# Kernel optimization log

Hardware: AMD Instinct MI355X
Metric: run time of the kernel (lower is better)

Reference implementation:

```python
import math
import jax, jax.numpy as jnp
import numpy as np

IMAGE_SIZE = 224


def _resize_bilinear(img, out_h, out_w):
    """PyTorch F.interpolate(mode='bilinear', align_corners=False) equivalent.
    img: [B, H, W] -> [B, out_h, out_w]. No antialiasing (matches torch default)."""
    B, H, W = img.shape

    def coords(out, size):
        r = jnp.maximum((jnp.arange(out, dtype=jnp.float32) + 0.5) * (size / out) - 0.5, 0.0)
        i0 = jnp.minimum(jnp.floor(r).astype(jnp.int32), size - 1)
        i1 = jnp.minimum(i0 + 1, size - 1)
        w = r - i0.astype(jnp.float32)
        return i0, i1, w

    r0, r1, wr = coords(out_h, H)
    c0, c1, wc = coords(out_w, W)
    rows = img[:, r0, :] * (1.0 - wr)[None, :, None] + img[:, r1, :] * wr[None, :, None]
    out = rows[:, :, c0] * (1.0 - wc)[None, None, :] + rows[:, :, c1] * wc[None, None, :]
    return out


def _normalize_minmax(x, eps=1e-8):
    mn = x.min()
    mx = x.max()
    return jnp.where(mx - mn < eps, jnp.zeros_like(x), (x - mn) / (mx - mn + eps))


def _grid_embed(vals, n):
    """Row-major scatter of vals[:, :n] into a ceil(sqrt(n))^2 grid (zero padded)."""
    B = vals.shape[0]
    gs = int(math.ceil(math.sqrt(n)))
    pad = gs * gs - n
    return jnp.pad(vals, ((0, 0), (0, pad))).reshape(B, gs, gs)


def setup_inputs() -> dict:
    key = jax.random.key(0)
    hidden_state = jax.random.normal(key, (32, 512, 4096, 1), dtype=jnp.float32)
    return {"hidden_state": hidden_state}


def reference(hidden_state):
    B, E, N, _ = hidden_state.shape
    x = hidden_state[..., 0]  # [B, E, N]

    # temporal view: mean over nodes -> [B, E] -> grid -> resize
    t_grid = _grid_embed(x.mean(axis=2), E)
    temporal = _normalize_minmax(_resize_bilinear(t_grid, IMAGE_SIZE, IMAGE_SIZE))

    # spatial view: mean over embedding dim -> [B, N] -> grid -> resize
    s_grid = _grid_embed(x.mean(axis=1), N)
    spatial = _normalize_minmax(_resize_bilinear(s_grid, IMAGE_SIZE, IMAGE_SIZE))

    # correlation view: row-normalized centered features, [B, E, E] correlation
    xc = x - x.mean(axis=2, keepdims=True)
    xn = xc / (jnp.linalg.norm(xc, axis=2, keepdims=True) + 1e-8)
    corr = jnp.einsum('bin,bjn->bij', xn, xn)  # [B, E, E]
    correlation = _normalize_minmax(_resize_bilinear(corr, IMAGE_SIZE, IMAGE_SIZE))

    # [B, 3, image_size, image_size]
    return jnp.stack([temporal, spatial, correlation], axis=1)
```

## Files before the change

### kernel.cpp

```cpp
#include <hip/hip_runtime.h>
#include <hip/hip_bf16.h>
#include <math.h>

#define IMG 224
#define PIX (IMG*IMG)
#define B_ 32
#define E_ 512
#define N_ 4096
#define SV_BLOCKS 256

typedef __attribute__((ext_vector_type(8))) short bf16x8;
typedef __attribute__((ext_vector_type(4))) float f32x4;

__device__ inline unsigned short f2bf(float f){
  unsigned u = __float_as_uint(f);
  unsigned r = (u + 0x7FFFu + ((u >> 16) & 1u)) >> 16;
  return (unsigned short)r;
}
__device__ inline float wave_sum(float v){
  #pragma unroll
  for (int o = 32; o; o >>= 1) v += __shfl_down(v, o);
  return v;
}

__global__ void __launch_bounds__(256) stats_fused(const float* __restrict__ x,
                                                   float* __restrict__ meanv,
                                                   float* __restrict__ rnormv,
                                                   float* __restrict__ colpart){
  int b = blockIdx.x >> 4, chunk = blockIdx.x & 15;
  int e0 = chunk << 5;
  const float* xb = x + ((size_t)b * E_ + e0) * N_;
  int t = threadIdx.x;
  float csum[16];
  #pragma unroll
  for (int k = 0; k < 16; k++) csum[k] = 0.f;
  __shared__ float red[16];
  float4 v[4];
  const float4* xr0 = (const float4*)xb;
  #pragma unroll
  for (int k = 0; k < 4; k++) v[k] = xr0[t + 256 * k];
  for (int e = 0; e < 32; e++){
    float s = 0.f, ss = 0.f;
    #pragma unroll
    for (int k = 0; k < 4; k++){
      float4 w = v[k];
      csum[4*k+0] += w.x; csum[4*k+1] += w.y;
      csum[4*k+2] += w.z; csum[4*k+3] += w.w;
      s  += w.x + w.y + w.z + w.w;
      ss += w.x*w.x + w.y*w.y + w.z*w.z + w.w*w.w;
    }
    if (e < 31){
      const float4* nx = (const float4*)(xb + (size_t)(e + 1) * N_);
      #pragma unroll
      for (int k = 0; k < 4; k++) v[k] = nx[t + 256 * k];
    }
    float sw = wave_sum(s), ssw = wave_sum(ss);
    int wv = t >> 6, ln = t & 63;
    __syncthreads();
    if (ln == 0){ red[wv] = sw; red[8 + wv] = ssw; }
    __syncthreads();
    if (t == 0){
      float S  = red[0] + red[1] + red[2] + red[3];
      float SS = red[8] + red[9] + red[10] + red[11];
      float mu = S * (1.f / N_);
      float var = fmaxf(SS - S * S * (1.f / N_), 0.f);
      meanv [b * E_ + e0 + e] = mu;
      rnormv[b * E_ + e0 + e] = 1.f / (sqrtf(var) + 1e-8f);
    }
  }
  float* cp = colpart + ((size_t)(b * 16 + chunk)) * N_;
  #pragma unroll
  for (int k = 0; k < 4; k++){
    float4 o;
    o.x = csum[4*k+0]; o.y = csum[4*k+1]; o.z = csum[4*k+2]; o.w = csum[4*k+3];
    *(float4*)(cp + 1024 * k + 4 * t) = o;
  }
}

__global__ void __launch_bounds__(256) col_finalize(const float* __restrict__ colpart,
                                                    float* __restrict__ colmean){
  int b = blockIdx.x >> 4;
  int n = ((blockIdx.x & 15) << 8) + threadIdx.x;
  float s = 0.f;
  #pragma unroll
  for (int c = 0; c < 16; c++) s += colpart[((size_t)(b * 16 + c)) * N_ + n];
  colmean[b * N_ + n] = s * (1.f / E_);
}

__device__ inline float grid_val(const float* v, int gs, int n, int r, int c){
  int idx = r * gs + c;
  return (idx < n) ? v[idx] : 0.f;
}
__device__ inline float bilin(const float* v, int gs, int n, int i, int j){
  float sc = (float)((double)gs / 224.0);
  float r = fmaxf(((float)i + 0.5f) * sc - 0.5f, 0.f);
  float c = fmaxf(((float)j + 0.5f) * sc - 0.5f, 0.f);
  int r0 = min((int)r, gs - 1), c0 = min((int)c, gs - 1);
  int r1 = min(r0 + 1, gs - 1), c1 = min(c0 + 1, gs - 1);
  float wr = r - (float)r0, wc = c - (float)c0;
  float v00 = grid_val(v, gs, n, r0, c0), v10 = grid_val(v, gs, n, r1, c0);
  float v01 = grid_val(v, gs, n, r0, c1), v11 = grid_val(v, gs, n, r1, c1);
  float ra = v00 * (1.f - wr) + v10 * wr;
  float rb = v01 * (1.f - wr) + v11 * wr;
  return ra * (1.f - wc) + rb * wc;
}

__global__ void __launch_bounds__(256) small_views(const float* __restrict__ meanv,
                                                   const float* __restrict__ colmean,
                                                   float* __restrict__ out,
                                                   float* __restrict__ scr){
  float tmn = INFINITY, tmx = -INFINITY, smn = INFINITY, smx = -INFINITY;
  for (int g = blockIdx.x * 256 + threadIdx.x; g < B_ * PIX; g += SV_BLOCKS * 256){
    int b = g / PIX, p = g - b * PIX;
    int i = p / IMG, j = p - i * IMG;
    float tv = bilin(meanv   + b * E_, 23, E_, i, j);
    float sv = bilin(colmean + b * N_, 64, N_, i, j);
    out[((size_t)b * 3 + 0) * PIX + p] = tv;
    out[((size_t)b * 3 + 1) * PIX + p] = sv;
    tmn = fminf(tmn, tv); tmx = fmaxf(tmx, tv);
    smn = fminf(smn, sv); smx = fmaxf(smx, sv);
  }
  #pragma unroll
  for (int o = 32; o; o >>= 1){
    tmn = fminf(tmn, __shfl_down(tmn, o)); tmx = fmaxf(tmx, __shfl_down(tmx, o));
    smn = fminf(smn, __shfl_down(smn, o)); smx = fmaxf(smx, __shfl_down(smx, o));
  }
  __shared__ float red[4][4];
  int wv = threadIdx.x >> 6, ln = threadIdx.x & 63;
  if (ln == 0){ red[wv][0] = tmn; red[wv][1] = tmx; red[wv][2] = smn; red[wv][3] = smx; }
  __syncthreads();
  if (threadIdx.x == 0){
    scr[blockIdx.x * 4 + 0] = fminf(fminf(red[0][0], red[1][0]), fminf(red[2][0], red[3][0]));
    scr[blockIdx.x * 4 + 1] = fmaxf(fmaxf(red[0][1], red[1][1]), fmaxf(red[2][1], red[3][1]));
    scr[blockIdx.x * 4 + 2] = fminf(fminf(red[0][2], red[1][2]), fminf(red[2][2], red[3][2]));
    scr[blockIdx.x * 4 + 3] = fmaxf(fmaxf(red[0][3], red[1][3]), fmaxf(red[2][3], red[3][3]));
  }
}

__global__ void __launch_bounds__(256) build_y(const float* __restrict__ x,
                                               const float* __restrict__ meanv,
                                               const float* __restrict__ rnormv,
                                               ushort* __restrict__ y, int b0){
  int bb = blockIdx.x / IMG;
  int i  = blockIdx.x % IMG;
  int b  = b0 + bb;
  float sc = (float)(512.0 / 224.0);
  float r = fmaxf(((float)i + 0.5f) * sc - 0.5f, 0.f);
  int r0 = min((int)r, E_ - 1);
  int r1 = min(r0 + 1, E_ - 1);
  float w = r - (float)r0;
  float rn0 = rnormv[b * E_ + r0], rn1 = rnormv[b * E_ + r1];
  float m0  = meanv [b * E_ + r0], m1  = meanv [b * E_ + r1];
  float a0 = (1.f - w) * rn0, a1 = w * rn1;
  float cc = -(a0 * m0 + a1 * m1);
  const float* x0 = x + ((size_t)b * E_ + r0) * N_;
  const float* x1 = x + ((size_t)b * E_ + r1) * N_;
  ushort* yo = y + ((size_t)bb * IMG + i) * N_;
  int c0 = threadIdx.x * 16;
  __align__(16) ushort tmp[16];
  #pragma unroll
  for (int q = 0; q < 4; q++){
    float4 v0 = *(const float4*)(x0 + c0 + q * 4);
    float4 v1 = *(const float4*)(x1 + c0 + q * 4);
    tmp[q * 4 + 0] = f2bf(a0 * v0.x + a1 * v1.x + cc);
    tmp[q * 4 + 1] = f2bf(a0 * v0.y + a1 * v1.y + cc);
    tmp[q * 4 + 2] = f2bf(a0 * v0.z + a1 * v1.z + cc);
    tmp[q * 4 + 3] = f2bf(a0 * v0.w + a1 * v1.w + cc);
  }
  *(int4*)(yo + c0)     = *(int4*)(tmp);
  *(int4*)(yo + c0 + 8) = *(int4*)(tmp + 8);
}

#define LDSTR 72
__global__ void __launch_bounds__(256) corr_gemm(const ushort* __restrict__ y,
                                                 float* __restrict__ out,
                                                 float* __restrict__ scr, int b0){
  int bb = blockIdx.x >> 4;
  int tile = blockIdx.x & 15;
  int ti = tile >> 2, tj = tile & 3;
  int b = b0 + bb;
  const ushort* yb = y + (size_t)bb * IMG * N_;
  __shared__ ushort lA[64 * LDSTR];
  __shared__ ushort lB[64 * LDSTR];
  int t = threadIdx.x;
  int wv = t >> 6, ln = t & 63;
  int wm = wv & 1, wn = wv >> 1;
  int quad = ln >> 4, l16 = ln & 15;
  f32x4 acc[2][2] = {};
  int s = t & 7, r2 = t >> 3;
  int rA0 = min(ti * 64 + r2,      223), rA1 = min(ti * 64 + r2 + 32, 223);
  int rB0 = min(tj * 64 + r2,      223), rB1 = min(tj * 64 + r2 + 32, 223);
  for (int k0 = 0; k0 < N_; k0 += 64){
    int4 a0 = *(const int4*)(yb + (size_t)rA0 * N_ + k0 + s * 8);
    int4 a1 = *(const int4*)(yb + (size_t)rA1 * N_ + k0 + s * 8);
    int4 b0v = *(const int4*)(yb + (size_t)rB0 * N_ + k0 + s * 8);
    int4 b1v = *(const int4*)(yb + (size_t)rB1 * N_ + k0 + s * 8);
    __syncthreads();
    *(int4*)(lA + r2 * LDSTR + s * 8)        = a0;
    *(int4*)(lA + (r2 + 32) * LDSTR + s * 8) = a1;
    *(int4*)(lB + r2 * LDSTR + s * 8)        = b0v;
    *(int4*)(lB + (r2 + 32) * LDSTR + s * 8) = b1v;
    __syncthreads();
    #pragma unroll
    for (int kk = 0; kk < 2; kk++){
      bf16x8 af0 = *(const bf16x8*)(lA + (wm * 32 + l16)      * LDSTR + kk * 32 + quad * 8);
      bf16x8 af1 = *(const bf16x8*)(lA + (wm * 32 + 16 + l16) * LDSTR + kk * 32 + quad * 8);
      bf16x8 bf0 = *(const bf16x8*)(lB + (wn * 32 + l16)      * LDSTR + kk * 32 + quad * 8);
      bf16x8 bf1 = *(const bf16x8*)(lB + (wn * 32 + 16 + l16) * LDSTR + kk * 32 + quad * 8);
      acc[0][0] = __builtin_amdgcn_mfma_f32_16x16x32_bf16(af0, bf0, acc[0][0], 0, 0, 0);
      acc[0][1] = __builtin_amdgcn_mfma_f32_16x16x32_bf16(af0, bf1, acc[0][1], 0, 0, 0);
      acc[1][0] = __builtin_amdgcn_mfma_f32_16x16x32_bf16(af1, bf0, acc[1][0], 0, 0, 0);
      acc[1][1] = __builtin_amdgcn_mfma_f32_16x16x32_bf16(af1, bf1, acc[1][1], 0, 0, 0);
    }
  }
  float mn = INFINITY, mx = -INFINITY;
  float* ov = out + ((size_t)b * 3 + 2) * PIX;
  #pragma unroll
  for (int im = 0; im < 2; im++)
    #pragma unroll
    for (int in = 0; in < 2; in++){
      #pragma unroll
      for (int rg = 0; rg < 4; rg++){
        int gi = ti * 64 + wm * 32 + im * 16 + quad * 4 + rg;
        int gj = tj * 64 + wn * 32 + in * 16 + l16;
        if (gi < IMG && gj < IMG){
          float v = acc[im][in][rg];
          ov[gi * IMG + gj] = v;
          mn = fminf(mn, v); mx = fmaxf(mx, v);
        }
      }
    }
  #pragma unroll
  for (int o = 32; o; o >>= 1){
    mn = fminf(mn, __shfl_down(mn, o)); mx = fmaxf(mx, __shfl_down(mx, o));
  }
  __shared__ float red[4][2];
  if (ln == 0){ red[wv][0] = mn; red[wv][1] = mx; }
  __syncthreads();
  if (t == 0){
    scr[(b * 16 + tile) * 2 + 0] = fminf(fminf(red[0][0], red[1][0]), fminf(red[2][0], red[3][0]));
    scr[(b * 16 + tile) * 2 + 1] = fmaxf(fmaxf(red[0][1], red[1][1]), fmaxf(red[2][1], red[3][1]));
  }
}

__global__ void __launch_bounds__(256) reduce_slots(const float* __restrict__ sv_scr,
                                                    const float* __restrict__ corr_scr,
                                                    float* __restrict__ slots){
  int t = threadIdx.x;
  float tmn = sv_scr[4*t+0], tmx = sv_scr[4*t+1];
  float smn = sv_scr[4*t+2], smx = sv_scr[4*t+3];
  float cmn = fminf(corr_scr[2*t],   corr_scr[2*(t+256)]);
  float cmx = fmaxf(corr_scr[2*t+1], corr_scr[2*(t+256)+1]);
  #pragma unroll
  for (int o = 32; o; o >>= 1){
    tmn = fminf(tmn, __shfl_down(tmn, o)); tmx = fmaxf(tmx, __shfl_down(tmx, o));
    smn = fminf(smn, __shfl_down(smn, o)); smx = fmaxf(smx, __shfl_down(smx, o));
    cmn = fminf(cmn, __shfl_down(cmn, o)); cmx = fmaxf(cmx, __shfl_down(cmx, o));
  }
  __shared__ float red[4][6];
  int wv = t >> 6, ln = t & 63;
  if (ln == 0){
    red[wv][0]=tmn; red[wv][1]=tmx; red[wv][2]=smn;
    red[wv][3]=smx; red[wv][4]=cmn; red[wv][5]=cmx;
  }
  __syncthreads();
  if (t == 0){
    slots[0] = fminf(fminf(red[0][0],red[1][0]), fminf(red[2][0],red[3][0]));
    slots[1] = fmaxf(fmaxf(red[0][1],red[1][1]), fmaxf(red[2][1],red[3][1]));
    slots[2] = fminf(fminf(red[0][2],red[1][2]), fminf(red[2][2],red[3][2]));
    slots[3] = fmaxf(fmaxf(red[0][3],red[1][3]), fmaxf(red[2][3],red[3][3]));
    slots[4] = fminf(fminf(red[0][4],red[1][4]), fminf(red[2][4],red[3][4]));
    slots[5] = fmaxf(fmaxf(red[0][5],red[1][5]), fmaxf(red[2][5],red[3][5]));
  }
}

__global__ void __launch_bounds__(256) normalize_k(float* __restrict__ out,
                                                   const float* __restrict__ slots){
  int g = blockIdx.x * 256 + threadIdx.x;
  if (g >= B_ * 3 * PIX) return;
  int view = (g / PIX) % 3;
  float mn = slots[2 * view];
  float mx = slots[2 * view + 1];
  float d = mx - mn;
  float v = out[g];
  out[g] = (d < 1e-8f) ? 0.f : (v - mn) / (d + 1e-8f);
}

extern "C" void kernel_launch(void* const* d_in, const int* in_sizes, int n_in,
                              void* d_out, int out_size, void* d_ws, size_t ws_size,
                              hipStream_t stream){
  const float* x = (const float*)d_in[0];
  float* out = (float*)d_out;
  char* ws = (char*)d_ws;
  float* slots    = (float*)(ws + 0);
  float* meanv    = (float*)(ws + 256);
  float* rnormv   = meanv + B_ * E_;
  float* colmean  = rnormv + B_ * E_;
  float* colpart  = colmean + B_ * N_;
  float* sv_scr   = colpart + (size_t)B_ * 16 * N_;
  float* corr_scr = sv_scr + SV_BLOCKS * 4;
  size_t y_off = ((size_t)((char*)(corr_scr + B_ * 16 * 2) - ws) + 255) & ~(size_t)255;
  ushort* y = (ushort*)(ws + y_off);
  int nb = B_;
  while (nb > 1 && y_off + (size_t)nb * IMG * N_ * 2 > ws_size) nb >>= 1;

  hipLaunchKernelGGL(stats_fused, dim3(B_ * 16), dim3(256), 0, stream,
                     x, meanv, rnormv, colpart);
  hipLaunchKernelGGL(col_finalize, dim3(B_ * 16), dim3(256), 0, stream,
                     colpart, colmean);
  hipLaunchKernelGGL(small_views, dim3(SV_BLOCKS), dim3(256), 0, stream,
                     meanv, colmean, out, sv_scr);
  for (int b0 = 0; b0 < B_; b0 += nb){
    hipLaunchKernelGGL(build_y, dim3(nb * IMG), dim3(256), 0, stream,
                       x, meanv, rnormv, y, b0);
    hipLaunchKernelGGL(corr_gemm, dim3(nb * 16), dim3(256), 0, stream,
                       y, out, corr_scr, b0);
  }
  hipLaunchKernelGGL(reduce_slots, dim3(1), dim3(256), 0, stream,
                     sv_scr, corr_scr, slots);
  hipLaunchKernelGGL(normalize_k, dim3((B_ * 3 * PIX + 255) / 256), dim3(256), 0, stream,
                     out, slots);
}
```

Baseline: 500.2 us.

## Fuse row stats with resized bf16 row build and exploit correlation symmetry

The row mean/norm statistics pass now also emits the row-interpolated, normalized bf16 matrix y while it streams x, so the separate build_y kernel and its second read of x (256 MB) are gone. Each block reads one extra row past its chunk so it can blend boundary pairs. The correlation GEMM computes only the upper-triangular 64x64 tiles (10 of 16 per batch) and writes each off-diagonal tile to both positions, using transposed float4 stores. The batch-chunking fallback for a small workspace is removed, so y must fit in full for all batches.

```diff
diff --git a/kernel.cpp b/kernel.cpp
--- a/kernel.cpp
+++ b/kernel.cpp
@@ -8,6 +8,7 @@
 #define E_ 512
 #define N_ 4096
 #define SV_BLOCKS 256
+#define SC_ ((float)(512.0/224.0))
 
 typedef __attribute__((ext_vector_type(8))) short bf16x8;
 typedef __attribute__((ext_vector_type(4))) float f32x4;
@@ -17,64 +18,83 @@
   unsigned r = (u + 0x7FFFu + ((u >> 16) & 1u)) >> 16;
   return (unsigned short)r;
 }
-__device__ inline float wave_sum(float v){
-  #pragma unroll
-  for (int o = 32; o; o >>= 1) v += __shfl_down(v, o);
-  return v;
-}
-
-__global__ void __launch_bounds__(256) stats_fused(const float* __restrict__ x,
-                                                   float* __restrict__ meanv,
-                                                   float* __restrict__ rnormv,
-                                                   float* __restrict__ colpart){
+
+__global__ void __launch_bounds__(256) stats_y(const float* __restrict__ x,
+                                               float* __restrict__ meanv,
+                                               float* __restrict__ colpart,
+                                               ushort* __restrict__ y){
   int b = blockIdx.x >> 4, chunk = blockIdx.x & 15;
   int e0 = chunk << 5;
-  const float* xb = x + ((size_t)b * E_ + e0) * N_;
   int t = threadIdx.x;
-  float csum[16];
-  #pragma unroll
-  for (int k = 0; k < 16; k++) csum[k] = 0.f;
-  __shared__ float red[16];
-  float4 v[4];
-  const float4* xr0 = (const float4*)xb;
-  #pragma unroll
-  for (int k = 0; k < 4; k++) v[k] = xr0[t + 256 * k];
-  for (int e = 0; e < 32; e++){
+  __shared__ short sInv[512];
+  __shared__ float sW[224];
+  __shared__ float red[2][16];
+  sInv[t] = -1; sInv[t + 256] = -1;
+  __syncthreads();
+  if (t < 224){
+    float r = fmaxf(((float)t + 0.5f) * SC_ - 0.5f, 0.f);
+    int r0 = min((int)r, E_ - 1);
+    sW[t] = r - (float)r0;
+    sInv[r0] = (short)t;
+  }
+  __syncthreads();
+
+  float cur[16], prev[16], nxt[16], csum[16];
+  #pragma unroll
+  for (int j = 0; j < 16; j++){ csum[j] = 0.f; prev[j] = 0.f; }
+  const float4* row0 = (const float4*)(x + ((size_t)b * E_ + e0) * N_);
+  #pragma unroll
+  for (int k = 0; k < 4; k++) *(float4*)(cur + 4 * k) = row0[4 * t + k];
+  float pmu = 0.f, prn = 0.f;
+
+  for (int idx = 0; idx <= 32; idx++){
+    int e = e0 + idx;
+    if (e >= E_) break;
+    bool hasNext = (idx < 32) && (e + 1 < E_);
+    if (hasNext){
+      const float4* nr = (const float4*)(x + ((size_t)b * E_ + e + 1) * N_);
+      #pragma unroll
+      for (int k = 0; k < 4; k++) *(float4*)(nxt + 4 * k) = nr[4 * t + k];
+    }
     float s = 0.f, ss = 0.f;
     #pragma unroll
-    for (int k = 0; k < 4; k++){
-      float4 w = v[k];
-      csum[4*k+0] += w.x; csum[4*k+1] += w.y;
-      csum[4*k+2] += w.z; csum[4*k+3] += w.w;
-      s  += w.x + w.y + w.z + w.w;
-      ss += w.x*w.x + w.y*w.y + w.z*w.z + w.w*w.w;
-    }
-    if (e < 31){
-      const float4* nx = (const float4*)(xb + (size_t)(e + 1) * N_);
+    for (int j = 0; j < 16; j++){ s += cur[j]; ss += cur[j] * cur[j]; }
+    #pragma unroll
+    for (int o = 32; o; o >>= 1){ s += __shfl_down(s, o); ss += __shfl_down(ss, o); }
+    int wv = t >> 6, ln = t & 63, p = idx & 1;
+    if (ln == 0){ red[p][wv] = s; red[p][8 + wv] = ss; }
+    __syncthreads();
+    float S  = red[p][0] + red[p][1] + red[p][2] + red[p][3];
+    float SS = red[p][8] + red[p][9] + red[p][10] + red[p][11];
+    float mu = S * (1.f / N_);
+    float var = fmaxf(SS - S * S * (1.f / N_), 0.f);
+    float rn = 1.f / (sqrtf(var) + 1e-8f);
+    if (idx < 32){
       #pragma unroll
-      for (int k = 0; k < 4; k++) v[k] = nx[t + 256 * k];
-    }
-    float sw = wave_sum(s), ssw = wave_sum(ss);
-    int wv = t >> 6, ln = t & 63;
-    __syncthreads();
-    if (ln == 0){ red[wv] = sw; red[8 + wv] = ssw; }
-    __syncthreads();
-    if (t == 0){
-      float S  = red[0] + red[1] + red[2] + red[3];
-      float SS = red[8] + red[9] + red[10] + red[11];
-      float mu = S * (1.f / N_);
-      float var = fmaxf(SS - S * S * (1.f / N_), 0.f);
-      meanv [b * E_ + e0 + e] = mu;
-      rnormv[b * E_ + e0 + e] = 1.f / (sqrtf(var) + 1e-8f);
-    }
-  }
-  float* cp = colpart + ((size_t)(b * 16 + chunk)) * N_;
-  #pragma unroll
-  for (int k = 0; k < 4; k++){
-    float4 o;
-    o.x = csum[4*k+0]; o.y = csum[4*k+1]; o.z = csum[4*k+2]; o.w = csum[4*k+3];
-    *(float4*)(cp + 1024 * k + 4 * t) = o;
-  }
+      for (int j = 0; j < 16; j++) csum[j] += cur[j];
+      if (t == 0) meanv[b * E_ + e] = mu;
+    }
+    if (idx >= 1){
+      int i = sInv[e - 1];
+      if (i >= 0){
+        float w = sW[i];
+        float a0 = (1.f - w) * prn, a1 = w * rn;
+        float cc = -(a0 * pmu + a1 * mu);
+        __align__(16) ushort tmp[16];
+        #pragma unroll
+        for (int j = 0; j < 16; j++) tmp[j] = f2bf(a0 * prev[j] + a1 * cur[j] + cc);
+        ushort* yo = y + ((size_t)b * IMG + i) * N_ + t * 16;
+        *(int4*)yo       = *(int4*)tmp;
+        *(int4*)(yo + 8) = *(int4*)(tmp + 8);
+      }
+    }
+    pmu = mu; prn = rn;
+    #pragma unroll
+    for (int j = 0; j < 16; j++){ prev[j] = cur[j]; if (hasNext) cur[j] = nxt[j]; }
+  }
+  float* cp = colpart + ((size_t)(b * 16 + chunk)) * N_ + t * 16;
+  #pragma unroll
+  for (int k = 0; k < 4; k++) *(float4*)(cp + 4 * k) = *(float4*)(csum + 4 * k);
 }
 
 __global__ void __launch_bounds__(256) col_finalize(const float* __restrict__ colpart,
@@ -137,49 +157,17 @@
   }
 }
 
-__global__ void __launch_bounds__(256) build_y(const float* __restrict__ x,
-                                               const float* __restrict__ meanv,
-                                               const float* __restrict__ rnormv,
-                                               ushort* __restrict__ y, int b0){
-  int bb = blockIdx.x / IMG;
-  int i  = blockIdx.x % IMG;
-  int b  = b0 + bb;
-  float sc = (float)(512.0 / 224.0);
-  float r = fmaxf(((float)i + 0.5f) * sc - 0.5f, 0.f);
-  int r0 = min((int)r, E_ - 1);
-  int r1 = min(r0 + 1, E_ - 1);
-  float w = r - (float)r0;
-  float rn0 = rnormv[b * E_ + r0], rn1 = rnormv[b * E_ + r1];
-  float m0  = meanv [b * E_ + r0], m1  = meanv [b * E_ + r1];
-  float a0 = (1.f - w) * rn0, a1 = w * rn1;
-  float cc = -(a0 * m0 + a1 * m1);
-  const float* x0 = x + ((size_t)b * E_ + r0) * N_;
-  const float* x1 = x + ((size_t)b * E_ + r1) * N_;
-  ushort* yo = y + ((size_t)bb * IMG + i) * N_;
-  int c0 = threadIdx.x * 16;
-  __align__(16) ushort tmp[16];
-  #pragma unroll
-  for (int q = 0; q < 4; q++){
-    float4 v0 = *(const float4*)(x0 + c0 + q * 4);
-    float4 v1 = *(const float4*)(x1 + c0 + q * 4);
-    tmp[q * 4 + 0] = f2bf(a0 * v0.x + a1 * v1.x + cc);
-    tmp[q * 4 + 1] = f2bf(a0 * v0.y + a1 * v1.y + cc);
-    tmp[q * 4 + 2] = f2bf(a0 * v0.z + a1 * v1.z + cc);
-    tmp[q * 4 + 3] = f2bf(a0 * v0.w + a1 * v1.w + cc);
-  }
-  *(int4*)(yo + c0)     = *(int4*)(tmp);
-  *(int4*)(yo + c0 + 8) = *(int4*)(tmp + 8);
-}
-
 #define LDSTR 72
 __global__ void __launch_bounds__(256) corr_gemm(const ushort* __restrict__ y,
                                                  float* __restrict__ out,
-                                                 float* __restrict__ scr, int b0){
-  int bb = blockIdx.x >> 4;
-  int tile = blockIdx.x & 15;
-  int ti = tile >> 2, tj = tile & 3;
-  int b = b0 + bb;
-  const ushort* yb = y + (size_t)bb * IMG * N_;
+                                                 float* __restrict__ scr){
+  const int TI[10] = {0,0,0,0,1,1,1,2,2,3};
+  const int TJ[10] = {0,1,2,3,1,2,3,2,3,3};
+  int b = blockIdx.x / 10;
+  int tile = blockIdx.x - b * 10;
+  int ti = TI[tile], tj = TJ[tile];
+  bool diag = (ti == tj);
+  const ushort* yb = y + (size_t)b * IMG * N_;
   __shared__ ushort lA[64 * LDSTR];
   __shared__ ushort lB[64 * LDSTR];
   int t = threadIdx.x;
@@ -219,16 +207,23 @@
   for (int im = 0; im < 2; im++)
     #pragma unroll
     for (int in = 0; in < 2; in++){
+      int gi0 = ti * 64 + wm * 32 + im * 16 + quad * 4;
+      int gj  = tj * 64 + wn * 32 + in * 16 + l16;
       #pragma unroll
       for (int rg = 0; rg < 4; rg++){
-        int gi = ti * 64 + wm * 32 + im * 16 + quad * 4 + rg;
-        int gj = tj * 64 + wn * 32 + in * 16 + l16;
+        int gi = gi0 + rg;
         if (gi < IMG && gj < IMG){
           float v = acc[im][in][rg];
           ov[gi * IMG + gj] = v;
           mn = fminf(mn, v); mx = fmaxf(mx, v);
         }
       }
+      if (!diag && gj < IMG && gi0 < IMG){
+        float4 tv;
+        tv.x = acc[im][in][0]; tv.y = acc[im][in][1];
+        tv.z = acc[im][in][2]; tv.w = acc[im][in][3];
+        *(float4*)(ov + gj * IMG + gi0) = tv;
+      }
     }
   #pragma unroll
   for (int o = 32; o; o >>= 1){
@@ -238,8 +233,8 @@
   if (ln == 0){ red[wv][0] = mn; red[wv][1] = mx; }
   __syncthreads();
   if (t == 0){
-    scr[(b * 16 + tile) * 2 + 0] = fminf(fminf(red[0][0], red[1][0]), fminf(red[2][0], red[3][0]));
-    scr[(b * 16 + tile) * 2 + 1] = fmaxf(fmaxf(red[0][1], red[1][1]), fmaxf(red[2][1], red[3][1]));
+    scr[(b * 10 + tile) * 2 + 0] = fminf(fminf(red[0][0], red[1][0]), fminf(red[2][0], red[3][0]));
+    scr[(b * 10 + tile) * 2 + 1] = fmaxf(fmaxf(red[0][1], red[1][1]), fmaxf(red[2][1], red[3][1]));
   }
 }
 
@@ -249,8 +244,11 @@
   int t = threadIdx.x;
   float tmn = sv_scr[4*t+0], tmx = sv_scr[4*t+1];
   float smn = sv_scr[4*t+2], smx = sv_scr[4*t+3];
-  float cmn = fminf(corr_scr[2*t],   corr_scr[2*(t+256)]);
-  float cmx = fmaxf(corr_scr[2*t+1], corr_scr[2*(t+256)+1]);
+  float cmn = INFINITY, cmx = -INFINITY;
+  for (int idx = t; idx < B_ * 10; idx += 256){
+    cmn = fminf(cmn, corr_scr[2*idx]);
+    cmx = fmaxf(cmx, corr_scr[2*idx+1]);
+  }
   #pragma unroll
   for (int o = 32; o; o >>= 1){
     tmn = fminf(tmn, __shfl_down(tmn, o)); tmx = fmaxf(tmx, __shfl_down(tmx, o));
@@ -294,28 +292,21 @@
   char* ws = (char*)d_ws;
   float* slots    = (float*)(ws + 0);
   float* meanv    = (float*)(ws + 256);
-  float* rnormv   = meanv + B_ * E_;
-  float* colmean  = rnormv + B_ * E_;
+  float* colmean  = meanv + B_ * E_;
   float* colpart  = colmean + B_ * N_;
   float* sv_scr   = colpart + (size_t)B_ * 16 * N_;
   float* corr_scr = sv_scr + SV_BLOCKS * 4;
-  size_t y_off = ((size_t)((char*)(corr_scr + B_ * 16 * 2) - ws) + 255) & ~(size_t)255;
+  size_t y_off = ((size_t)((char*)(corr_scr + B_ * 10 * 2) - ws) + 255) & ~(size_t)255;
   ushort* y = (ushort*)(ws + y_off);
-  int nb = B_;
-  while (nb > 1 && y_off + (size_t)nb * IMG * N_ * 2 > ws_size) nb >>= 1;
-
-  hipLaunchKernelGGL(stats_fused, dim3(B_ * 16), dim3(256), 0, stream,
-                     x, meanv, rnormv, colpart);
+
+  hipLaunchKernelGGL(stats_y, dim3(B_ * 16), dim3(256), 0, stream,
+                     x, meanv, colpart, y);
   hipLaunchKernelGGL(col_finalize, dim3(B_ * 16), dim3(256), 0, stream,
                      colpart, colmean);
   hipLaunchKernelGGL(small_views, dim3(SV_BLOCKS), dim3(256), 0, stream,
                      meanv, colmean, out, sv_scr);
-  for (int b0 = 0; b0 < B_; b0 += nb){
-    hipLaunchKernelGGL(build_y, dim3(nb * IMG), dim3(256), 0, stream,
-                       x, meanv, rnormv, y, b0);
-    hipLaunchKernelGGL(corr_gemm, dim3(nb * 16), dim3(256), 0, stream,
-                       y, out, corr_scr, b0);
-  }
+  hipLaunchKernelGGL(corr_gemm, dim3(B_ * 10), dim3(256), 0, stream,
+                     y, out, corr_scr);
   hipLaunchKernelGGL(reduce_slots, dim3(1), dim3(256), 0, stream,
                      sv_scr, corr_scr, slots);
   hipLaunchKernelGGL(normalize_k, dim3((B_ * 3 * PIX + 255) / 256), dim3(256), 0, stream,
```

After: 460.1 us. 8.0% less time.
